# Kernel tuning notes

Measured on AMD Instinct MI355X. Metric: run time of the kernel, lower is better.

Reference implementation:

```python
import jax, jax.numpy as jnp
import numpy as np

B = 8192          # batch
CIN = 256         # in_channels
COUT = 64         # out_channels
K = 3             # kernel_size
NK = 4            # num_kernels
HIDDEN = int(CIN * 0.25)   # attention hidden = int(in_channels*ratio) = 64
TEMP = 34.0       # attention temperature
KAN_IN = 64 * 4   # base*4 = flattened conv output (COUT*2*2)
GRID_SIZE, SPLINE_ORDER = 5, 3
GMIN, GMAX = -1.0, 1.0
NUM_BASES = GRID_SIZE + SPLINE_ORDER  # 8


def setup_inputs() -> dict:
    key = jax.random.key(0)
    ks = jax.random.split(key, 8)
    s = 0.05
    return {
        "x": jax.random.normal(ks[0], (B, CIN, 4, 4), jnp.float32),
        # dynamic-conv kernel bank [num_kernels, out, in, k, k]
        "weight": jax.random.normal(ks[1], (NK, COUT, CIN, K, K), jnp.float32) * s,
        "bias": jnp.zeros((NK, COUT), jnp.float32),
        # Attention2D: GAP -> fc1 (1x1 conv == linear) -> ReLU -> fc2 -> softmax(/T)
        "fc1_w": jax.random.normal(ks[2], (HIDDEN, CIN), jnp.float32) * s,
        "fc1_b": jnp.zeros((HIDDEN,), jnp.float32),
        "fc2_w": jax.random.normal(ks[3], (NK, HIDDEN), jnp.float32) * s,
        "fc2_b": jnp.zeros((NK,), jnp.float32),
        # KANLinear params (efficient-KAN style)
        "kan_base_w": jax.random.normal(ks[4], (COUT, KAN_IN), jnp.float32) * s,
        "kan_spline_w": jax.random.normal(ks[5], (COUT, KAN_IN, NUM_BASES), jnp.float32) * s,
        "kan_spline_scaler": jnp.ones((COUT, KAN_IN), jnp.float32),
    }


def _bspline_bases(x):
    """Cox-de Boor B-spline bases; x [B, F] -> [B, F, GRID_SIZE+SPLINE_ORDER]."""
    h = (GMAX - GMIN) / GRID_SIZE
    # extended grid, shared across features: length grid_size + 2*order + 1 = 12
    grid = jnp.arange(-SPLINE_ORDER, GRID_SIZE + SPLINE_ORDER + 1, dtype=x.dtype) * h + GMIN
    xe = x[..., None]  # [B, F, 1]
    bases = ((xe >= grid[:-1]) & (xe < grid[1:])).astype(x.dtype)  # order 0
    for k in range(1, SPLINE_ORDER + 1):
        left = (xe - grid[: -(k + 1)]) / (grid[k:-1] - grid[: -(k + 1)]) * bases[..., :-1]
        right = (grid[k + 1:] - xe) / (grid[k + 1:] - grid[1:-k]) * bases[..., 1:]
        bases = left + right
    return bases  # [B, F, 8]


def reference(x, weight, bias, fc1_w, fc1_b, fc2_w, fc2_b,
              kan_base_w, kan_spline_w, kan_spline_scaler):
    b = x.shape[0]
    # --- Attention2D: softmax over kernel bank ---
    pooled = x.mean(axis=(2, 3))                                  # [B, CIN]
    hid = jax.nn.relu(pooled @ fc1_w.T + fc1_b)                   # [B, HIDDEN]
    attn = jax.nn.softmax((hid @ fc2_w.T + fc2_b) / TEMP, axis=-1)  # [B, NK]
    # --- per-sample dynamic conv, fused form ---
    # sum_k a[b,k] * conv(x, W_k) == conv with per-sample aggregated weight
    w_all = weight.reshape(NK * COUT, CIN, K, K)
    y = jax.lax.conv_general_dilated(
        x, w_all, window_strides=(1, 1), padding="VALID",
        dimension_numbers=("NCHW", "OIHW", "NCHW"))                # [B, NK*COUT, 2, 2]
    y = y.reshape(b, NK, COUT, y.shape[-2], y.shape[-1])
    conv_out = jnp.einsum("bk,bkohw->bohw", attn, y)
    conv_out = conv_out + (attn @ bias)[:, :, None, None]          # aggregated bias
    # --- KANLinear on flattened conv output ---
    feat = conv_out.reshape(b, -1)                                 # [B, 256]
    base_out = jax.nn.silu(feat) @ kan_base_w.T                    # [B, COUT]
    bases = _bspline_bases(feat)                                   # [B, 256, 8]
    spline_out = jnp.einsum("big,oig->bo", bases,
                            kan_spline_w * kan_spline_scaler[..., None])
    return base_out + spline_out                                   # [B, COUT]
```

## Files before the change

kernel.cpp:

```cpp
#include <hip/hip_runtime.h>

#define BT   8192
#define MS   16
#define XBUF (MS * 656)

typedef _Float16 half8  __attribute__((ext_vector_type(8)));
typedef _Float16 half4v __attribute__((ext_vector_type(4)));
typedef float    floatx4  __attribute__((ext_vector_type(4)));
typedef float    floatx16 __attribute__((ext_vector_type(16)));

__global__ __launch_bounds__(256) void w3_transform(
    const float* __restrict__ weight, _Float16* __restrict__ W3)
{
    const int n = blockIdx.x;
    const int c = threadIdx.x;
    const float* src = weight + ((size_t)n * 256 + c) * 9;
    const int cc = c >> 5, ci = c & 31;
    #pragma unroll
    for (int ij = 0; ij < 9; ++ij) {
        W3[((size_t)(cc * 9 + ij) * 256 + n) * 32 + ci] = (_Float16)src[ij];
    }
}

__global__ __launch_bounds__(256) void wk3_transform(
    const float* __restrict__ base_w, const float* __restrict__ spline_w,
    const float* __restrict__ scaler, const float* __restrict__ fc1_w,
    _Float16* __restrict__ Wk3, _Float16* __restrict__ Wf3)
{
    const int st = blockIdx.x;
    const int tid = threadIdx.x;
    if (st < 72) {
        #pragma unroll
        for (int u = 0; u < 8; ++u) {
            const int idx = u * 256 + tid;
            const int n = idx >> 5, kk = idx & 31;
            const int k = st * 32 + kk;
            float v;
            if (k < 256) {
                v = base_w[n * 256 + k];
            } else {
                const int r = k - 256;
                const int i = r >> 3, g = r & 7;
                v = spline_w[((size_t)n * 256 + i) * 8 + g] * scaler[n * 256 + i];
            }
            Wk3[(size_t)st * 2048 + idx] = (_Float16)v;
        }
    } else {
        const int st2 = st - 72;
        #pragma unroll
        for (int u = 0; u < 8; ++u) {
            const int idx = u * 256 + tid;
            const int n = idx >> 5, kk = idx & 31;
            Wf3[(size_t)st2 * 2048 + idx] = (_Float16)fc1_w[n * 256 + st2 * 32 + kk];
        }
    }
}

__device__ __forceinline__ void bases8c(float xv, _Float16* dst) {
    const float t = (xv + 2.2f) * 2.5f;
    const float ft = floorf(t);
    const int idx = (int)ft;
    const float u = t - ft, v = 1.f - u;
    const float u2 = u * u, v2 = v * v;
    const float c3 = u2 * u * (1.f / 6.f);
    const float c2 = (1.f / 6.f) + 0.5f * (u + u2 - u2 * u);
    const float c1 = (1.f / 6.f) + 0.5f * (v + v2 - v2 * v);
    const float c0 = v2 * v * (1.f / 6.f);
    half8 hb;
    #pragma unroll
    for (int tt = 0; tt < 8; ++tt) {
        const int d = idx - tt;
        float b = 0.f;
        b = (d == 0) ? c3 : b;
        b = (d == 1) ? c2 : b;
        b = (d == 2) ? c1 : b;
        b = (d == 3) ? c0 : b;
        hb[tt] = (_Float16)b;
    }
    *(half8*)dst = hb;
}

__global__ __launch_bounds__(512, 4) void fused_kernel(
    const float* __restrict__ x, const _Float16* __restrict__ W3,
    const _Float16* __restrict__ Wk3, const _Float16* __restrict__ Wf3,
    const float* __restrict__ bias, const float* __restrict__ fc1_b,
    const float* __restrict__ fc2_w, const float* __restrict__ fc2_b,
    float* __restrict__ out)
{
    __shared__ __align__(16) char smem[MS * 2312 * 2];
    __shared__ float hid_lds[MS * 68];
    __shared__ float attn_s[MS][4];

    _Float16* Xs  = (_Float16*)smem;
    _Float16* Pl  = (_Float16*)(smem + 2 * XBUF * 2);
    _Float16* Act = (_Float16*)smem;

    const int tid = threadIdx.x;
    const int wv = tid >> 6, lane = tid & 63;
    const int nl = lane & 15, q = lane >> 4;
    const int cg = wv & 3, rh = wv >> 2;
    const int b0 = blockIdx.x * MS;

    const int posr = nl & 3;
    const int aLane = (nl >> 2) * 656 + ((posr >> 1) * 4 + (posr & 1)) * 40 + q * 8;
    const int lbW0 = (((rh * 2 + 0) * 4 + cg) * 16 + nl) * 32 + q * 8;
    const int lbW1 = (((rh * 2 + 1) * 4 + cg) * 16 + nl) * 32 + q * 8;

    const int s_ = tid >> 5, cch = tid & 31;
    const float* xg = x + ((size_t)(b0 + s_) * 256 + cch) * 16;

    floatx4 acc[4][2];
    #pragma unroll
    for (int rt = 0; rt < 4; ++rt) {
        acc[rt][0] = floatx4{0.f, 0.f, 0.f, 0.f};
        acc[rt][1] = floatx4{0.f, 0.f, 0.f, 0.f};
    }

    floatx16 r = *(const floatx16*)xg;
    {
        _Float16* xd = &Xs[s_ * 656 + cch];
        #pragma unroll
        for (int p = 0; p < 16; ++p) xd[p * 40] = (_Float16)r[p];
        float sm = 0.f;
        #pragma unroll
        for (int p = 0; p < 16; ++p) sm += r[p];
        Pl[s_ * 264 + cch] = (_Float16)(sm * (1.0f / 16.0f));
    }
    r = *(const floatx16*)(xg + 512);
    __syncthreads();

    #pragma unroll 1
    for (int cc = 0; cc < 8; ++cc) {
        const int cur = cc & 1;
        if (cc < 7) {
            _Float16* xd = &Xs[(cur ^ 1) * XBUF + s_ * 656 + cch];
            #pragma unroll
            for (int p = 0; p < 16; ++p) xd[p * 40] = (_Float16)r[p];
            float sm = 0.f;
            #pragma unroll
            for (int p = 0; p < 16; ++p) sm += r[p];
            Pl[s_ * 264 + (cc + 1) * 32 + cch] = (_Float16)(sm * (1.0f / 16.0f));
        }
        if (cc < 6) r = *(const floatx16*)(xg + (cc + 2) * 512);

        const _Float16* wst = W3 + (size_t)cc * 9 * 8192;
        const _Float16* xb = &Xs[cur * XBUF + aLane];
        half8 bA0 = *(const half8*)(wst + lbW0);
        half8 bB0 = *(const half8*)(wst + lbW1);
        half8 bA1 = *(const half8*)(wst + 8192 + lbW0);
        half8 bB1 = *(const half8*)(wst + 8192 + lbW1);
        #pragma unroll
        for (int ij = 0; ij < 9; ++ij) {
            half8 bA2, bB2;
            if (ij < 7) {
                bA2 = *(const half8*)(wst + (ij + 2) * 8192 + lbW0);
                bB2 = *(const half8*)(wst + (ij + 2) * 8192 + lbW1);
            }
            const int p0 = (ij / 3) * 4 + (ij % 3);
            half8 aF[4];
            #pragma unroll
            for (int rt = 0; rt < 4; ++rt)
                aF[rt] = *(const half8*)&xb[rt * 2624 + p0 * 40];
            #pragma unroll
            for (int rt = 0; rt < 4; ++rt) {
                acc[rt][0] = __builtin_amdgcn_mfma_f32_16x16x32_f16(aF[rt], bA0, acc[rt][0], 0, 0, 0);
                acc[rt][1] = __builtin_amdgcn_mfma_f32_16x16x32_f16(aF[rt], bB0, acc[rt][1], 0, 0, 0);
            }
            bA0 = bA1; bB0 = bB1; bA1 = bA2; bB1 = bB2;
        }
        __syncthreads();
    }

    if (rh == 0) {
        floatx4 a1 = floatx4{0.f, 0.f, 0.f, 0.f};
        const _Float16* wfb = Wf3 + ((cg * 16 + nl) * 32 + q * 8);
        const _Float16* pb = &Pl[nl * 264 + q * 8];
        #pragma unroll
        for (int st = 0; st < 8; ++st) {
            const half8 aF = *(const half8*)(pb + st * 32);
            const half8 bF = *(const half8*)(wfb + st * 2048);
            a1 = __builtin_amdgcn_mfma_f32_16x16x32_f16(aF, bF, a1, 0, 0, 0);
        }
        const int h = cg * 16 + nl;
        const float fb = fc1_b[h];
        #pragma unroll
        for (int reg = 0; reg < 4; ++reg)
            hid_lds[(q * 4 + reg) * 68 + h] = fmaxf(a1[reg] + fb, 0.f);
    }
    __syncthreads();

    if (wv == 0) {
        const int s = lane >> 2, kb = lane & 3;
        float l = fc2_b[kb];
        #pragma unroll 8
        for (int h = 0; h < 64; ++h) l += hid_lds[s * 68 + h] * fc2_w[kb * 64 + h];
        float m = fmaxf(l, __shfl_xor(l, 1));
        m = fmaxf(m, __shfl_xor(m, 2));
        const float e = __expf((l - m) * (1.0f / 34.0f));
        float sm = e + __shfl_xor(e, 1);
        sm += __shfl_xor(sm, 2);
        attn_s[s][kb] = e / sm;
    }
    __syncthreads();

    const int o = cg * 16 + nl;
    if (rh == 1) {
        #pragma unroll
        for (int rt = 0; rt < 4; ++rt) {
            const int s = rt * 4 + q;
            const float a2w = attn_s[s][2], a3w = attn_s[s][3];
            #pragma unroll
            for (int e = 0; e < 4; ++e) {
                float* slot = (float*)&Act[s * 2312 + 256 + (o * 4 + e) * 8];
                slot[0] = a2w * acc[rt][0][e] + a3w * acc[rt][1][e];
            }
        }
    }
    __syncthreads();

    if (rh == 0) {
        const float bb0 = bias[o], bb1 = bias[64 + o], bb2 = bias[128 + o], bb3 = bias[192 + o];
        #pragma unroll
        for (int rt = 0; rt < 4; ++rt) {
            const int s = rt * 4 + q;
            const float a0 = attn_s[s][0], a1 = attn_s[s][1],
                        a2 = attn_s[s][2], a3 = attn_s[s][3];
            const float badd = a0 * bb0 + a1 * bb1 + a2 * bb2 + a3 * bb3;
            float f[4];
            #pragma unroll
            for (int e = 0; e < 4; ++e) {
                const float part = ((float*)&Act[s * 2312 + 256 + (o * 4 + e) * 8])[0];
                f[e] = a0 * acc[rt][0][e] + a1 * acc[rt][1][e] + part + badd;
            }
            half4v sv;
            #pragma unroll
            for (int e = 0; e < 4; ++e) {
                const float ex = __expf(-f[e]);
                sv[e] = (_Float16)(f[e] * __builtin_amdgcn_rcpf(1.f + ex));
            }
            *(half4v*)&Act[s * 2312 + o * 4] = sv;
            #pragma unroll
            for (int e = 0; e < 4; ++e)
                bases8c(f[e], &Act[s * 2312 + 256 + (o * 4 + e) * 8]);
        }
    }
    __syncthreads();

    {
        floatx4 a2 = floatx4{0.f, 0.f, 0.f, 0.f};
        const _Float16* wkb = Wk3 + ((size_t)(cg * 16 + nl) * 32 + q * 8);
        const _Float16* ab = &Act[nl * 2312 + q * 8];
        const int st0 = rh * 36;
        half8 kb0 = *(const half8*)(wkb + (size_t)st0 * 2048);
        half8 kb1 = *(const half8*)(wkb + (size_t)(st0 + 1) * 2048);
        #pragma unroll 4
        for (int i = 0; i < 36; ++i) {
            half8 kb2;
            if (i < 34) kb2 = *(const half8*)(wkb + (size_t)(st0 + i + 2) * 2048);
            const half8 aF = *(const half8*)(ab + (st0 + i) * 32);
            a2 = __builtin_amdgcn_mfma_f32_16x16x32_f16(aF, kb0, a2, 0, 0, 0);
            kb0 = kb1; kb1 = kb2;
        }
        if (rh == 1) *(floatx4*)&hid_lds[cg * 256 + lane * 4] = a2;
        __syncthreads();
        if (rh == 0) {
            const floatx4 p = *(const floatx4*)&hid_lds[cg * 256 + lane * 4];
            a2 = a2 + p;
            #pragma unroll
            for (int reg = 0; reg < 4; ++reg)
                out[(size_t)(b0 + q * 4 + reg) * 64 + cg * 16 + nl] = a2[reg];
        }
    }
}

extern "C" void kernel_launch(void* const* d_in, const int* in_sizes, int n_in,
                              void* d_out, int out_size, void* d_ws, size_t ws_size,
                              hipStream_t stream) {
    const float* x          = (const float*)d_in[0];
    const float* weight     = (const float*)d_in[1];
    const float* bias       = (const float*)d_in[2];
    const float* fc1_w      = (const float*)d_in[3];
    const float* fc1_b      = (const float*)d_in[4];
    const float* fc2_w      = (const float*)d_in[5];
    const float* fc2_b      = (const float*)d_in[6];
    const float* kan_base_w = (const float*)d_in[7];
    const float* kan_spline = (const float*)d_in[8];
    const float* kan_scaler = (const float*)d_in[9];
    float* out = (float*)d_out;

    _Float16* W3  = (_Float16*)d_ws;
    _Float16* Wk3 = W3 + (size_t)72 * 8192;
    _Float16* Wf3 = Wk3 + (size_t)72 * 2048;

    w3_transform<<<256, 256, 0, stream>>>(weight, W3);
    wk3_transform<<<80, 256, 0, stream>>>(kan_base_w, kan_spline, kan_scaler,
                                          fc1_w, Wk3, Wf3);
    fused_kernel<<<BT / MS, 512, 0, stream>>>(x, W3, Wk3, Wf3, bias, fc1_b,
                                              fc2_w, fc2_b, out);
}
```

Baseline: 251.0 us.

## Split conv taps across wave halves and merge prep kernels into one launch

```diff
diff --git a/kernel.cpp b/kernel.cpp
--- a/kernel.cpp
+++ b/kernel.cpp
@@ -9,27 +9,26 @@
 typedef float    floatx4  __attribute__((ext_vector_type(4)));
 typedef float    floatx16 __attribute__((ext_vector_type(16)));
 
-__global__ __launch_bounds__(256) void w3_transform(
-    const float* __restrict__ weight, _Float16* __restrict__ W3)
+__global__ __launch_bounds__(256) void prep_kernel(
+    const float* __restrict__ weight, const float* __restrict__ base_w,
+    const float* __restrict__ spline_w, const float* __restrict__ scaler,
+    const float* __restrict__ fc1_w,
+    _Float16* __restrict__ W3, _Float16* __restrict__ Wk3,
+    _Float16* __restrict__ Wf3)
 {
-    const int n = blockIdx.x;
-    const int c = threadIdx.x;
-    const float* src = weight + ((size_t)n * 256 + c) * 9;
-    const int cc = c >> 5, ci = c & 31;
-    #pragma unroll
-    for (int ij = 0; ij < 9; ++ij) {
-        W3[((size_t)(cc * 9 + ij) * 256 + n) * 32 + ci] = (_Float16)src[ij];
-    }
-}
-
-__global__ __launch_bounds__(256) void wk3_transform(
-    const float* __restrict__ base_w, const float* __restrict__ spline_w,
-    const float* __restrict__ scaler, const float* __restrict__ fc1_w,
-    _Float16* __restrict__ Wk3, _Float16* __restrict__ Wf3)
-{
-    const int st = blockIdx.x;
+    const int bb = blockIdx.x;
     const int tid = threadIdx.x;
-    if (st < 72) {
+    if (bb < 256) {
+        const int n = bb;
+        const int c = tid;
+        const float* src = weight + ((size_t)n * 256 + c) * 9;
+        const int cc = c >> 5, ci = c & 31;
+        #pragma unroll
+        for (int ij = 0; ij < 9; ++ij) {
+            W3[((size_t)(cc * 9 + ij) * 256 + n) * 32 + ci] = (_Float16)src[ij];
+        }
+    } else if (bb < 328) {
+        const int st = bb - 256;
         #pragma unroll
         for (int u = 0; u < 8; ++u) {
             const int idx = u * 256 + tid;
@@ -46,7 +45,7 @@
             Wk3[(size_t)st * 2048 + idx] = (_Float16)v;
         }
     } else {
-        const int st2 = st - 72;
+        const int st2 = bb - 328;
         #pragma unroll
         for (int u = 0; u < 8; ++u) {
             const int idx = u * 256 + tid;
@@ -98,22 +97,29 @@
     const int tid = threadIdx.x;
     const int wv = tid >> 6, lane = tid & 63;
     const int nl = lane & 15, q = lane >> 4;
-    const int cg = wv & 3, rh = wv >> 2;
+    const int cg = wv & 3, kh = wv >> 2;
     const int b0 = blockIdx.x * MS;
 
     const int posr = nl & 3;
     const int aLane = (nl >> 2) * 656 + ((posr >> 1) * 4 + (posr & 1)) * 40 + q * 8;
-    const int lbW0 = (((rh * 2 + 0) * 4 + cg) * 16 + nl) * 32 + q * 8;
-    const int lbW1 = (((rh * 2 + 1) * 4 + cg) * 16 + nl) * 32 + q * 8;
+    const int lbW = (cg * 16 + nl) * 32 + q * 8;
 
     const int s_ = tid >> 5, cch = tid & 31;
     const float* xg = x + ((size_t)(b0 + s_) * 256 + cch) * 16;
 
-    floatx4 acc[4][2];
+    floatx4 acc[4][4];
     #pragma unroll
-    for (int rt = 0; rt < 4; ++rt) {
-        acc[rt][0] = floatx4{0.f, 0.f, 0.f, 0.f};
-        acc[rt][1] = floatx4{0.f, 0.f, 0.f, 0.f};
+    for (int rt = 0; rt < 4; ++rt)
+        #pragma unroll
+        for (int kb = 0; kb < 4; ++kb)
+            acc[rt][kb] = floatx4{0.f, 0.f, 0.f, 0.f};
+
+    half8 bcur[4];
+    {
+        const _Float16* w0 = W3 + (size_t)(kh ? 5 : 0) * 8192 + lbW;
+        #pragma unroll
+        for (int kb = 0; kb < 4; ++kb)
+            bcur[kb] = *(const half8*)(w0 + kb * 2048);
     }
 
     floatx16 r = *(const floatx16*)xg;
@@ -143,35 +149,79 @@
         }
         if (cc < 6) r = *(const floatx16*)(xg + (cc + 2) * 512);
 
-        const _Float16* wst = W3 + (size_t)cc * 9 * 8192;
+        const _Float16* wst = W3 + (size_t)cc * 9 * 8192 + lbW;
         const _Float16* xb = &Xs[cur * XBUF + aLane];
-        half8 bA0 = *(const half8*)(wst + lbW0);
-        half8 bB0 = *(const half8*)(wst + lbW1);
-        half8 bA1 = *(const half8*)(wst + 8192 + lbW0);
-        half8 bB1 = *(const half8*)(wst + 8192 + lbW1);
-        #pragma unroll
-        for (int ij = 0; ij < 9; ++ij) {
-            half8 bA2, bB2;
-            if (ij < 7) {
-                bA2 = *(const half8*)(wst + (ij + 2) * 8192 + lbW0);
-                bB2 = *(const half8*)(wst + (ij + 2) * 8192 + lbW1);
-            }
-            const int p0 = (ij / 3) * 4 + (ij % 3);
-            half8 aF[4];
-            #pragma unroll
-            for (int rt = 0; rt < 4; ++rt)
-                aF[rt] = *(const half8*)&xb[rt * 2624 + p0 * 40];
-            #pragma unroll
-            for (int rt = 0; rt < 4; ++rt) {
-                acc[rt][0] = __builtin_amdgcn_mfma_f32_16x16x32_f16(aF[rt], bA0, acc[rt][0], 0, 0, 0);
-                acc[rt][1] = __builtin_amdgcn_mfma_f32_16x16x32_f16(aF[rt], bB0, acc[rt][1], 0, 0, 0);
-            }
-            bA0 = bA1; bB0 = bB1; bA1 = bA2; bB1 = bB2;
+
+        #pragma unroll
+        for (int i = 0; i < 4; ++i) {
+            const int ijn = (i < 3) ? (kh ? 6 + i : 1 + i) : 4;
+            half8 bnxt[4];
+            #pragma unroll
+            for (int kb = 0; kb < 4; ++kb)
+                bnxt[kb] = *(const half8*)(wst + (size_t)ijn * 8192 + kb * 2048);
+
+            const int p0 = kh ? ((int[4]){6, 8, 9, 10})[i]
+                              : ((int[4]){0, 1, 2, 4})[i];
+
+            {
+                const half8 aF0 = *(const half8*)&xb[0 * 2624 + p0 * 40];
+                const half8 aF1 = *(const half8*)&xb[1 * 2624 + p0 * 40];
+                #pragma unroll
+                for (int kb = 0; kb < 4; ++kb)
+                    acc[0][kb] = __builtin_amdgcn_mfma_f32_16x16x32_f16(aF0, bcur[kb], acc[0][kb], 0, 0, 0);
+                #pragma unroll
+                for (int kb = 0; kb < 4; ++kb)
+                    acc[1][kb] = __builtin_amdgcn_mfma_f32_16x16x32_f16(aF1, bcur[kb], acc[1][kb], 0, 0, 0);
+            }
+            {
+                const half8 aF2 = *(const half8*)&xb[2 * 2624 + p0 * 40];
+                const half8 aF3 = *(const half8*)&xb[3 * 2624 + p0 * 40];
+                #pragma unroll
+                for (int kb = 0; kb < 4; ++kb)
+                    acc[2][kb] = __builtin_amdgcn_mfma_f32_16x16x32_f16(aF2, bcur[kb], acc[2][kb], 0, 0, 0);
+                #pragma unroll
+                for (int kb = 0; kb < 4; ++kb)
+                    acc[3][kb] = __builtin_amdgcn_mfma_f32_16x16x32_f16(aF3, bcur[kb], acc[3][kb], 0, 0, 0);
+            }
+            #pragma unroll
+            for (int kb = 0; kb < 4; ++kb) bcur[kb] = bnxt[kb];
+        }
+
+        {
+            const _Float16* wnx = (cc < 7)
+                ? (W3 + (size_t)(cc + 1) * 9 * 8192 + (size_t)(kh ? 5 : 0) * 8192 + lbW)
+                : (W3 + lbW);
+            half8 bnxt[4];
+            #pragma unroll
+            for (int kb = 0; kb < 4; ++kb)
+                bnxt[kb] = *(const half8*)(wnx + kb * 2048);
+
+            if (kh == 0) {
+                const half8 aF0 = *(const half8*)&xb[0 * 2624 + 5 * 40];
+                const half8 aF1 = *(const half8*)&xb[1 * 2624 + 5 * 40];
+                #pragma unroll
+                for (int kb = 0; kb < 4; ++kb)
+                    acc[0][kb] = __builtin_amdgcn_mfma_f32_16x16x32_f16(aF0, bcur[kb], acc[0][kb], 0, 0, 0);
+                #pragma unroll
+                for (int kb = 0; kb < 4; ++kb)
+                    acc[1][kb] = __builtin_amdgcn_mfma_f32_16x16x32_f16(aF1, bcur[kb], acc[1][kb], 0, 0, 0);
+            } else {
+                const half8 aF2 = *(const half8*)&xb[2 * 2624 + 5 * 40];
+                const half8 aF3 = *(const half8*)&xb[3 * 2624 + 5 * 40];
+                #pragma unroll
+                for (int kb = 0; kb < 4; ++kb)
+                    acc[2][kb] = __builtin_amdgcn_mfma_f32_16x16x32_f16(aF2, bcur[kb], acc[2][kb], 0, 0, 0);
+                #pragma unroll
+                for (int kb = 0; kb < 4; ++kb)
+                    acc[3][kb] = __builtin_amdgcn_mfma_f32_16x16x32_f16(aF3, bcur[kb], acc[3][kb], 0, 0, 0);
+            }
+            #pragma unroll
+            for (int kb = 0; kb < 4; ++kb) bcur[kb] = bnxt[kb];
         }
         __syncthreads();
     }
 
-    if (rh == 0) {
+    if (kh == 0) {
         floatx4 a1 = floatx4{0.f, 0.f, 0.f, 0.f};
         const _Float16* wfb = Wf3 + ((cg * 16 + nl) * 32 + q * 8);
         const _Float16* pb = &Pl[nl * 264 + q * 8];
@@ -204,21 +254,23 @@
     __syncthreads();
 
     const int o = cg * 16 + nl;
-    if (rh == 1) {
+    if (kh == 1) {
         #pragma unroll
         for (int rt = 0; rt < 4; ++rt) {
             const int s = rt * 4 + q;
-            const float a2w = attn_s[s][2], a3w = attn_s[s][3];
+            const float a0 = attn_s[s][0], a1 = attn_s[s][1],
+                        a2 = attn_s[s][2], a3 = attn_s[s][3];
             #pragma unroll
             for (int e = 0; e < 4; ++e) {
                 float* slot = (float*)&Act[s * 2312 + 256 + (o * 4 + e) * 8];
-                slot[0] = a2w * acc[rt][0][e] + a3w * acc[rt][1][e];
-            }
-        }
-    }
-    __syncthreads();
-
-    if (rh == 0) {
+                slot[0] = a0 * acc[rt][0][e] + a1 * acc[rt][1][e]
+                        + a2 * acc[rt][2][e] + a3 * acc[rt][3][e];
+            }
+        }
+    }
+    __syncthreads();
+
+    if (kh == 0) {
         const float bb0 = bias[o], bb1 = bias[64 + o], bb2 = bias[128 + o], bb3 = bias[192 + o];
         #pragma unroll
         for (int rt = 0; rt < 4; ++rt) {
@@ -230,7 +282,8 @@
             #pragma unroll
             for (int e = 0; e < 4; ++e) {
                 const float part = ((float*)&Act[s * 2312 + 256 + (o * 4 + e) * 8])[0];
-                f[e] = a0 * acc[rt][0][e] + a1 * acc[rt][1][e] + part + badd;
+                f[e] = a0 * acc[rt][0][e] + a1 * acc[rt][1][e]
+                     + a2 * acc[rt][2][e] + a3 * acc[rt][3][e] + part + badd;
             }
             half4v sv;
             #pragma unroll
@@ -250,7 +303,7 @@
         floatx4 a2 = floatx4{0.f, 0.f, 0.f, 0.f};
         const _Float16* wkb = Wk3 + ((size_t)(cg * 16 + nl) * 32 + q * 8);
         const _Float16* ab = &Act[nl * 2312 + q * 8];
-        const int st0 = rh * 36;
+        const int st0 = kh * 36;
         half8 kb0 = *(const half8*)(wkb + (size_t)st0 * 2048);
         half8 kb1 = *(const half8*)(wkb + (size_t)(st0 + 1) * 2048);
         #pragma unroll 4
@@ -261,9 +314,9 @@
             a2 = __builtin_amdgcn_mfma_f32_16x16x32_f16(aF, kb0, a2, 0, 0, 0);
             kb0 = kb1; kb1 = kb2;
         }
-        if (rh == 1) *(floatx4*)&hid_lds[cg * 256 + lane * 4] = a2;
+        if (kh == 1) *(floatx4*)&hid_lds[cg * 256 + lane * 4] = a2;
         __syncthreads();
-        if (rh == 0) {
+        if (kh == 0) {
             const floatx4 p = *(const floatx4*)&hid_lds[cg * 256 + lane * 4];
             a2 = a2 + p;
             #pragma unroll
@@ -292,9 +345,8 @@
     _Float16* Wk3 = W3 + (size_t)72 * 8192;
     _Float16* Wf3 = Wk3 + (size_t)72 * 2048;
 
-    w3_transform<<<256, 256, 0, stream>>>(weight, W3);
-    wk3_transform<<<80, 256, 0, stream>>>(kan_base_w, kan_spline, kan_scaler,
-                                          fc1_w, Wk3, Wf3);
+    prep_kernel<<<336, 256, 0, stream>>>(weight, kan_base_w, kan_spline,
+                                         kan_scaler, fc1_w, W3, Wk3, Wf3);
     fused_kernel<<<BT / MS, 512, 0, stream>>>(x, W3, Wk3, Wf3, bias, fc1_b,
                                               fc2_w, fc2_b, out);
 }
```

New measurement: 284.2 us. +13.2%, slower.
